# Kernel optimization log

Measured on AMD Instinct MI355X. Metric: run time of the kernel, lower is better.

## Reference

```python
import jax, jax.numpy as jnp
import numpy as np

HIDDEN = 1024


def setup_inputs() -> dict:
    key = jax.random.key(0)
    ks = jax.random.split(key, 8)
    x_in, y_in, out_dim, hidden = 1024, 1024, 1024, HIDDEN
    Nx, Ny = 4096, 4096
    s = lambda d: 1.0 / np.sqrt(d)
    return {
        "x": jax.random.normal(ks[0], (Nx, x_in), jnp.float32),
        "y": jax.random.normal(ks[1], (Ny, y_in), jnp.float32),
        "Wq": jax.random.normal(ks[2], (hidden, x_in), jnp.float32) * s(x_in),
        "bq": jnp.zeros((hidden,), jnp.float32),
        "Wk": jax.random.normal(ks[3], (hidden, y_in), jnp.float32) * s(y_in),
        "bk": jnp.zeros((hidden,), jnp.float32),
        "Wv": jax.random.normal(ks[4], (out_dim, y_in), jnp.float32) * s(y_in),
        "bv": jnp.zeros((out_dim,), jnp.float32),
    }


def reference(x, y, Wq, bq, Wk, bk, Wv, bv):
    # Linear projections (torch Linear: x @ W.T + b)
    q = x @ Wq.T + bq          # [Nx, H]
    k = y @ Wk.T + bk          # [Ny, H]
    v = y @ Wv.T + bv          # [Ny, D_out]
    scores = (q @ k.T) / jnp.sqrt(jnp.asarray(HIDDEN, q.dtype))  # [Nx, Ny]
    attn = jax.nn.softmax(scores, axis=1)
    return attn @ v            # [Nx, D_out]
```

## Files before the change

### kernel.cpp

```cpp
#include <hip/hip_runtime.h>
#include <cstdint>
#include <cstddef>

typedef __attribute__((ext_vector_type(8))) __bf16 bf16x8;
typedef __attribute__((ext_vector_type(4))) float  f32x4;

#define WAITCNT_VM(n) ((n & 0xF) | 0x70 | 0xF00 | (((n) >> 4) << 14))
#define WAITCNT_LGKM0 (0xF | 0x70 | (3 << 14))

__device__ __forceinline__ unsigned short f32_to_bf16(float f) {
    union { float f; unsigned int u; } cv;
    cv.f = f;
    unsigned int u = cv.u;
    return (unsigned short)((u + 0x7fffu + ((u >> 16) & 1u)) >> 16);
}

__device__ __forceinline__ float bf16_to_f32(unsigned short h) {
    union { unsigned int u; float f; } cv;
    cv.u = ((unsigned int)h) << 16;
    return cv.f;
}

__device__ __forceinline__ void async_copy16(const unsigned short* g, unsigned short* lds) {
    __builtin_amdgcn_global_load_lds(
        (const __attribute__((address_space(1))) unsigned int*)g,
        (__attribute__((address_space(3))) unsigned int*)lds,
        16, 0, 0);
}

__global__ __launch_bounds__(256) void cast_all(
    const float* __restrict__ x,  const float* __restrict__ y,
    const float* __restrict__ wq, const float* __restrict__ wk, const float* __restrict__ wv,
    unsigned short* __restrict__ xb,  unsigned short* __restrict__ yb,
    unsigned short* __restrict__ wqb, unsigned short* __restrict__ wkb,
    unsigned short* __restrict__ wvb, float* __restrict__ lsum)
{
    int b = blockIdx.x;
    if (b >= 11264) {
        float4 z = {0.f, 0.f, 0.f, 0.f};
#pragma unroll
        for (int t = 0; t < 4; ++t)
            ((float4*)lsum)[threadIdx.x * 4 + t] = z;
        return;
    }
    const float* s; unsigned short* d; int base;
    if      (b < 4096)  { s = x;  d = xb;  base = b; }
    else if (b < 8192)  { s = y;  d = yb;  base = b - 4096; }
    else if (b < 9216)  { s = wq; d = wqb; base = b - 8192; }
    else if (b < 10240) { s = wk; d = wkb; base = b - 9216; }
    else                { s = wv; d = wvb; base = b - 10240; }
    int i = base * 256 + threadIdx.x;
    float4 v = ((const float4*)s)[i];
    ushort4 o;
    o.x = f32_to_bf16(v.x);
    o.y = f32_to_bf16(v.y);
    o.z = f32_to_bf16(v.z);
    o.w = f32_to_bf16(v.w);
    ((ushort4*)d)[i] = o;
}

__device__ __forceinline__ void gemm_core_pf(
    const unsigned short* __restrict__ A, const unsigned short* __restrict__ B,
    int K, int rowBase, int colBase, int kBeg, int kEnd,
    unsigned short* ldsA, unsigned short* ldsB, f32x4 acc[4][4])
{
    const int tid  = threadIdx.x;
    const int lane = tid & 63;
    const int wave = tid >> 6;
    const int quad = lane >> 4;
    const int r    = lane & 15;
    const int wm   = wave >> 1;
    const int wn   = wave & 1;

    const int c1 = tid + 256;
    const long aOff0 = (long)(rowBase + (tid >> 2)) * K + (tid & 3) * 8;
    const long aOff1 = (long)(rowBase + (c1  >> 2)) * K + (c1  & 3) * 8;
    const long bOff0 = (long)(colBase + (tid >> 2)) * K + (tid & 3) * 8;
    const long bOff1 = (long)(colBase + (c1  >> 2)) * K + (c1  & 3) * 8;
    unsigned short* ldsA0 = ldsA + tid * 8;
    unsigned short* ldsA1 = ldsA + c1 * 8;
    unsigned short* ldsB0 = ldsB + tid * 8;
    unsigned short* ldsB1 = ldsB + c1 * 8;

    const int aReadOff = (wm * 64 + r) * 32 + quad * 8;
    const int bReadOff = (wn * 64 + r) * 32 + quad * 8;

    const int nSteps = (kEnd - kBeg) >> 5;

    async_copy16(A + aOff0 + kBeg, ldsA0);
    async_copy16(A + aOff1 + kBeg, ldsA1);
    async_copy16(B + bOff0 + kBeg, ldsB0);
    async_copy16(B + bOff1 + kBeg, ldsB1);

    for (int s = 0; s < nSteps; ++s) {
        const int cur = (s & 1) << 12;
        const int nxt = cur ^ 4096;
        __builtin_amdgcn_s_waitcnt(0);
        __syncthreads();
        if (s + 1 < nSteps) {
            const int kn = kBeg + ((s + 1) << 5);
            async_copy16(A + aOff0 + kn, ldsA0 + nxt);
            async_copy16(A + aOff1 + kn, ldsA1 + nxt);
            async_copy16(B + bOff0 + kn, ldsB0 + nxt);
            async_copy16(B + bOff1 + kn, ldsB1 + nxt);
        }
        bf16x8 af[4], bfr[4];
#pragma unroll
        for (int i = 0; i < 4; ++i)
            af[i] = *(const bf16x8*)(ldsA + cur + aReadOff + i * 16 * 32);
#pragma unroll
        for (int j = 0; j < 4; ++j)
            bfr[j] = *(const bf16x8*)(ldsB + cur + bReadOff + j * 16 * 32);
#pragma unroll
        for (int i = 0; i < 4; ++i)
#pragma unroll
            for (int j = 0; j < 4; ++j)
                acc[i][j] = __builtin_amdgcn_mfma_f32_16x16x32_bf16(af[i], bfr[j], acc[i][j], 0, 0, 0);
    }
}

__global__ __launch_bounds__(256, 2)
void proj_batched(const unsigned short* __restrict__ xb, const unsigned short* __restrict__ yb,
                  const unsigned short* __restrict__ wqb, const unsigned short* __restrict__ wkb,
                  const unsigned short* __restrict__ wvb,
                  unsigned short* __restrict__ q, unsigned short* __restrict__ k,
                  unsigned short* __restrict__ vt,
                  const float* __restrict__ bq, const float* __restrict__ bk,
                  const float* __restrict__ bv)
{
    __shared__ __align__(16) unsigned short ldsA[2 * 128 * 32];
    __shared__ __align__(16) unsigned short ldsB[2 * 128 * 32];

    const int b = blockIdx.x;
    const int z = b >> 8;
    const int rb = b & 255;

    const unsigned short *A, *B;
    unsigned short* C;
    const float* bias;
    int N, rowBase, colBase;
    bool biasPerRow;
    if (z == 0) {
        A = xb; B = wqb; C = q; bias = bq; N = 1024; biasPerRow = false;
        colBase = (rb >> 5) * 128; rowBase = (rb & 31) * 128;
    } else if (z == 1) {
        A = yb; B = wkb; C = k; bias = bk; N = 1024; biasPerRow = false;
        colBase = (rb >> 5) * 128; rowBase = (rb & 31) * 128;
    } else {
        A = wvb; B = yb; C = vt; bias = bv; N = 4096; biasPerRow = true;
        colBase = (rb >> 3) * 128; rowBase = (rb & 7) * 128;
    }

    f32x4 acc[4][4];
#pragma unroll
    for (int i = 0; i < 4; ++i)
#pragma unroll
        for (int j = 0; j < 4; ++j)
            acc[i][j] = (f32x4){0.f, 0.f, 0.f, 0.f};

    gemm_core_pf(A, B, 1024, rowBase, colBase, 0, 1024, ldsA, ldsB, acc);

    const int lane = threadIdx.x & 63;
    const int wave = threadIdx.x >> 6;
    const int quad = lane >> 4;
    const int r    = lane & 15;
    const int orow0 = rowBase + (wave >> 1) * 64 + quad * 4;
    const int ocol0 = colBase + (wave & 1) * 64 + r;

#pragma unroll
    for (int i = 0; i < 4; ++i)
#pragma unroll
        for (int e = 0; e < 4; ++e) {
            const int row = orow0 + i * 16 + e;
            const float brow = biasPerRow ? bias[row] : 0.f;
#pragma unroll
            for (int j = 0; j < 4; ++j) {
                const int col = ocol0 + j * 16;
                const float bb = biasPerRow ? brow : bias[col];
                C[(long)row * N + col] = f32_to_bf16(acc[i][j][e] + bb);
            }
        }
}

__device__ __forceinline__ void stage_half(const unsigned short* src, long rstep,
                                           unsigned short* ldsLane) {
    async_copy16(src, ldsLane);
    async_copy16(src + rstep, ldsLane + 4096);
}

__device__ __forceinline__ void gemm256_core(
    const unsigned short* __restrict__ A, const unsigned short* __restrict__ B,
    int K, int rowBase, int colBase, int kBeg, int nTiles,
    unsigned short* lds, f32x4 acc[8][4])
{
    const int tid  = threadIdx.x;
    const int lane = tid & 63;
    const int wid  = tid >> 6;
    const int quad = lane >> 4;
    const int r    = lane & 15;
    const int wm   = wid >> 2;
    const int wn   = wid & 3;

    const int row0 = tid >> 3;
    const int chs8 = (((tid & 7) ^ (row0 & 7)) << 3);
    const unsigned short* As = A + (long)(rowBase + row0) * K + chs8 + kBeg;
    const unsigned short* Bs = B + (long)(colBase + row0) * K + chs8 + kBeg;
    const long rstep = (long)K * 64;
    const long hstep = (long)K * 128;
    unsigned short* ldsLane = lds + tid * 8;

    const int aRd = (wm << 13) + (r << 6);
    const int bRd = 16384 + (wn << 12) + (r << 6);
    const int sw0 = ((quad ^ (r & 7)) << 3);
    const int sw1 = (((quad + 4) ^ (r & 7)) << 3);

    stage_half(As,         rstep, ldsLane);
    stage_half(As + hstep, rstep, ldsLane + 8192);
    stage_half(Bs,         rstep, ldsLane + 16384);
    stage_half(Bs + hstep, rstep, ldsLane + 24576);
    if (nTiles > 1) {
        stage_half(As + 64,         rstep, ldsLane + 32768);
        stage_half(As + hstep + 64, rstep, ldsLane + 40960);
    }
    __builtin_amdgcn_s_waitcnt(WAITCNT_VM(4));
    __builtin_amdgcn_s_barrier();
    __builtin_amdgcn_sched_barrier(0);

    for (int T = 0; T < nTiles; ++T) {
        const int cur = (T & 1) << 15;
        const int nxt = cur ^ 32768;

        bf16x8 a0[8], b0[4];
        if (T + 1 < nTiles) stage_half(Bs + (T + 1) * 64, rstep, ldsLane + nxt + 16384);
#pragma unroll
        for (int i = 0; i < 8; ++i)
            a0[i] = *(const bf16x8*)(lds + cur + aRd + i * 1024 + sw0);
#pragma unroll
        for (int j = 0; j < 4; ++j)
            b0[j] = *(const bf16x8*)(lds + cur + bRd + j * 1024 + sw0);
        __builtin_amdgcn_s_barrier();
        __builtin_amdgcn_s_waitcnt(WAITCNT_LGKM0);
        __builtin_amdgcn_sched_barrier(0);
        __builtin_amdgcn_s_setprio(1);
#pragma unroll
        for (int i = 0; i < 4; ++i)
#pragma unroll
            for (int j = 0; j < 4; ++j)
                acc[i][j] = __builtin_amdgcn_mfma_f32_16x16x32_bf16(a0[i], b0[j], acc[i][j], 0, 0, 0);
        __builtin_amdgcn_s_setprio(0);
        __builtin_amdgcn_s_barrier();

        if (T + 1 < nTiles) stage_half(Bs + hstep + (T + 1) * 64, rstep, ldsLane + nxt + 24576);
        __builtin_amdgcn_s_setprio(1);
#pragma unroll
        for (int i = 4; i < 8; ++i)
#pragma unroll
            for (int j = 0; j < 4; ++j)
                acc[i][j] = __builtin_amdgcn_mfma_f32_16x16x32_bf16(a0[i], b0[j], acc[i][j], 0, 0, 0);
        __builtin_amdgcn_s_setprio(0);
        __builtin_amdgcn_s_barrier();

        bf16x8 a1[8], b1[4];
#pragma unroll
        for (int i = 0; i < 8; ++i)
            a1[i] = *(const bf16x8*)(lds + cur + aRd + i * 1024 + sw1);
#pragma unroll
        for (int j = 0; j < 4; ++j)
            b1[j] = *(const bf16x8*)(lds + cur + bRd + j * 1024 + sw1);
        __builtin_amdgcn_s_barrier();
        __builtin_amdgcn_s_waitcnt(WAITCNT_LGKM0);
        __builtin_amdgcn_sched_barrier(0);
        __builtin_amdgcn_s_setprio(1);
#pragma unroll
        for (int i = 0; i < 4; ++i)
#pragma unroll
            for (int j = 0; j < 4; ++j)
                acc[i][j] = __builtin_amdgcn_mfma_f32_16x16x32_bf16(a1[i], b1[j], acc[i][j], 0, 0, 0);
        __builtin_amdgcn_s_setprio(0);
        __builtin_amdgcn_s_barrier();

        if (T + 2 < nTiles) {
            stage_half(As + (T + 2) * 64,         rstep, ldsLane + cur);
            stage_half(As + hstep + (T + 2) * 64, rstep, ldsLane + cur + 8192);
        }
        __builtin_amdgcn_s_setprio(1);
#pragma unroll
        for (int i = 4; i < 8; ++i)
#pragma unroll
            for (int j = 0; j < 4; ++j)
                acc[i][j] = __builtin_amdgcn_mfma_f32_16x16x32_bf16(a1[i], b1[j], acc[i][j], 0, 0, 0);
        __builtin_amdgcn_s_setprio(0);

        if (T + 2 < nTiles) __builtin_amdgcn_s_waitcnt(WAITCNT_VM(4));
        else                __builtin_amdgcn_s_waitcnt(WAITCNT_VM(0));
        __builtin_amdgcn_s_barrier();
        __builtin_amdgcn_sched_barrier(0);
    }
}

__global__ __launch_bounds__(512, 2)
void scores_gemm256(const unsigned short* __restrict__ q, const unsigned short* __restrict__ k,
                    unsigned short* __restrict__ P, float* __restrict__ lsum, float scale2)
{
    __shared__ __align__(16) unsigned short lds[2 * 32768];

    const int bid = blockIdx.x;
    const int swz = (bid & 7) * 32 + (bid >> 3);
    const int mt = swz >> 4, nt = swz & 15;
    const int rowBase = mt * 256;
    const int colBase = nt * 256;

    f32x4 acc[8][4];
#pragma unroll
    for (int i = 0; i < 8; ++i)
#pragma unroll
        for (int j = 0; j < 4; ++j)
            acc[i][j] = (f32x4){0.f, 0.f, 0.f, 0.f};

    gemm256_core(q, k, 1024, rowBase, colBase, 0, 16, lds, acc);

    const int lane = threadIdx.x & 63;
    const int wid  = threadIdx.x >> 6;
    const int quad = lane >> 4;
    const int r    = lane & 15;
    const int orow0 = rowBase + (wid >> 2) * 128 + quad * 4;
    const int ocol0 = colBase + (wid & 3) * 64 + r;

#pragma unroll
    for (int mi = 0; mi < 8; ++mi)
#pragma unroll
        for (int e = 0; e < 4; ++e) {
            const int row = orow0 + mi * 16 + e;
            float rs = 0.f;
#pragma unroll
            for (int nj = 0; nj < 4; ++nj) {
                const float p = exp2f(acc[mi][nj][e] * scale2);
                rs += p;
                P[(long)row * 4096 + ocol0 + nj * 16] = f32_to_bf16(p);
            }
#pragma unroll
            for (int m = 1; m < 16; m <<= 1) rs += __shfl_xor(rs, m, 64);
            if (r == 0) atomicAdd(&lsum[row], rs);
        }
}

template <int ATOMIC>
__global__ __launch_bounds__(512, 2)
void out_gemm256(const unsigned short* __restrict__ P, const unsigned short* __restrict__ vt,
                 void* __restrict__ Out)
{
    __shared__ __align__(16) unsigned short lds[2 * 32768];

    const int bid = blockIdx.x;
    const int swz = (bid & 7) * 32 + (bid >> 3);
    const int z  = swz & 3;
    const int nt = (swz >> 2) & 3;
    const int mt = swz >> 4;
    const int rowBase = mt * 256;
    const int colBase = nt * 256;
    const int kBeg = z * 1024;

    f32x4 acc[8][4];
#pragma unroll
    for (int i = 0; i < 8; ++i)
#pragma unroll
        for (int j = 0; j < 4; ++j)
            acc[i][j] = (f32x4){0.f, 0.f, 0.f, 0.f};

    gemm256_core(P, vt, 4096, rowBase, colBase, kBeg, 16, lds, acc);

    const int lane = threadIdx.x & 63;
    const int wid  = threadIdx.x >> 6;
    const int quad = lane >> 4;
    const int r    = lane & 15;
    const int orow0 = rowBase + (wid >> 2) * 128 + quad * 4;
    const int ocol0 = colBase + (wid & 3) * 64 + r;

#pragma unroll
    for (int mi = 0; mi < 8; ++mi)
#pragma unroll
        for (int e = 0; e < 4; ++e) {
            const int row = orow0 + mi * 16 + e;
#pragma unroll
            for (int nj = 0; nj < 4; ++nj) {
                const int col = ocol0 + nj * 16;
                if (ATOMIC) {
                    atomicAdd(&((float*)Out)[(long)row * 1024 + col], acc[mi][nj][e]);
                } else {
                    unsigned short* parts = (unsigned short*)Out + (size_t)z * (4096 * 1024);
                    parts[(long)row * 1024 + col] = f32_to_bf16(acc[mi][nj][e]);
                }
            }
        }
}

__global__ __launch_bounds__(256) void reduce_norm4(const unsigned short* __restrict__ parts,
                                                    const float* __restrict__ lsum,
                                                    float* __restrict__ O) {
    const int i = blockIdx.x * 256 + threadIdx.x;
    const float inv = 1.0f / lsum[i >> 8];
    const size_t stride = (size_t)(4096 * 1024) / 4;
    ushort4 a = ((const ushort4*)parts)[i];
    ushort4 b = ((const ushort4*)parts)[i + stride];
    ushort4 c = ((const ushort4*)parts)[i + 2 * stride];
    ushort4 d = ((const ushort4*)parts)[i + 3 * stride];
    float4 o;
    o.x = (bf16_to_f32(a.x) + bf16_to_f32(b.x) + bf16_to_f32(c.x) + bf16_to_f32(d.x)) * inv;
    o.y = (bf16_to_f32(a.y) + bf16_to_f32(b.y) + bf16_to_f32(c.y) + bf16_to_f32(d.y)) * inv;
    o.z = (bf16_to_f32(a.z) + bf16_to_f32(b.z) + bf16_to_f32(c.z) + bf16_to_f32(d.z)) * inv;
    o.w = (bf16_to_f32(a.w) + bf16_to_f32(b.w) + bf16_to_f32(c.w) + bf16_to_f32(d.w)) * inv;
    ((float4*)O)[i] = o;
}

__global__ __launch_bounds__(256) void norm_rows(float* __restrict__ O, const float* __restrict__ lsum) {
    int i = blockIdx.x * 256 + threadIdx.x;
    const float inv = 1.0f / lsum[i >> 8];
    float4 v = ((const float4*)O)[i];
    v.x *= inv; v.y *= inv; v.z *= inv; v.w *= inv;
    ((float4*)O)[i] = v;
}

extern "C" void kernel_launch(void* const* d_in, const int* in_sizes, int n_in,
                              void* d_out, int out_size, void* d_ws, size_t ws_size,
                              hipStream_t stream) {
    const float* x  = (const float*)d_in[0];
    const float* y  = (const float*)d_in[1];
    const float* Wq = (const float*)d_in[2];
    const float* bq = (const float*)d_in[3];
    const float* Wk = (const float*)d_in[4];
    const float* bk = (const float*)d_in[5];
    const float* Wv = (const float*)d_in[6];
    const float* bv = (const float*)d_in[7];

    constexpr int Nx = 4096, Ny = 4096, H = 1024, Dv = 1024, Kin = 1024;

    char* ws = (char*)d_ws;
    size_t off = 0;
    auto carve = [&](size_t bytes) {
        char* p = ws + off;
        off += (bytes + 255) & ~(size_t)255;
        return p;
    };

    unsigned short* q_bf  = (unsigned short*)carve((size_t)Nx * H * 2);
    unsigned short* k_bf  = (unsigned short*)carve((size_t)Ny * H * 2);
    unsigned short* vt_bf = (unsigned short*)carve((size_t)Dv * Ny * 2);
    float*          lsum  = (float*)carve((size_t)Nx * sizeof(float));

    char* overlay = ws + off;
    unsigned short* x_bf  = (unsigned short*)overlay;
    unsigned short* y_bf  = x_bf  + (size_t)Nx * Kin;
    unsigned short* Wq_bf = y_bf  + (size_t)Ny * Kin;
    unsigned short* Wk_bf = Wq_bf + (size_t)H  * Kin;
    unsigned short* Wv_bf = Wk_bf + (size_t)H  * Kin;
    unsigned short* P_bf  = (unsigned short*)overlay;

    const size_t overlay_bytes = (size_t)Nx * Ny * 2;
    const size_t partsBytes = (size_t)Nx * Dv * 2;
    unsigned short* parts = (unsigned short*)(overlay + overlay_bytes);
    const size_t need_parts = (size_t)((overlay + overlay_bytes + 4 * partsBytes) - ws);
    const bool useParts = ws_size >= need_parts;

    if (!useParts)
        hipMemsetAsync(d_out, 0, (size_t)Nx * Dv * sizeof(float), stream);

    cast_all<<<11265, 256, 0, stream>>>(x, y, Wq, Wk, Wv, x_bf, y_bf, Wq_bf, Wk_bf, Wv_bf, lsum);

    proj_batched<<<768, 256, 0, stream>>>(x_bf, y_bf, Wq_bf, Wk_bf, Wv_bf,
                                          q_bf, k_bf, vt_bf, bq, bk, bv);

    const float scale2 = 1.4426950408889634f / 32.0f;
    scores_gemm256<<<256, 512, 0, stream>>>(q_bf, k_bf, P_bf, lsum, scale2);

    if (useParts) {
        out_gemm256<0><<<256, 512, 0, stream>>>(P_bf, vt_bf, parts);
        reduce_norm4<<<(Nx * Dv / 4) / 256, 256, 0, stream>>>(parts, lsum, (float*)d_out);
    } else {
        out_gemm256<1><<<256, 512, 0, stream>>>(P_bf, vt_bf, d_out);
        norm_rows<<<Nx * Dv / 4 / 256, 256, 0, stream>>>((float*)d_out, lsum);
    }
}
```

Measured before the change: 223.4 us.

## Restructure GEMM mainloop to overlap LDS fragment reads with MFMA clusters

```diff
diff --git a/kernel.cpp b/kernel.cpp
--- a/kernel.cpp
+++ b/kernel.cpp
@@ -5,8 +5,8 @@
 typedef __attribute__((ext_vector_type(8))) __bf16 bf16x8;
 typedef __attribute__((ext_vector_type(4))) float  f32x4;
 
-#define WAITCNT_VM(n) ((n & 0xF) | 0x70 | 0xF00 | (((n) >> 4) << 14))
-#define WAITCNT_LGKM0 (0xF | 0x70 | (3 << 14))
+#define WAITCNT_VM(n)   ((n & 0xF) | 0x70 | 0xF00 | (((n) >> 4) << 14))
+#define WAITCNT_LGKM(n) (0xF | 0x70 | ((n) << 8) | (3 << 14))
 
 __device__ __forceinline__ unsigned short f32_to_bf16(float f) {
     union { float f; unsigned int u; } cv;
@@ -219,82 +219,101 @@
     stage_half(Bs,         rstep, ldsLane + 16384);
     stage_half(Bs + hstep, rstep, ldsLane + 24576);
     if (nTiles > 1) {
-        stage_half(As + 64,         rstep, ldsLane + 32768);
-        stage_half(As + hstep + 64, rstep, ldsLane + 40960);
+        stage_half(Bs + 64,         rstep, ldsLane + 32768 + 16384);
+        stage_half(Bs + hstep + 64, rstep, ldsLane + 32768 + 24576);
     }
     __builtin_amdgcn_s_waitcnt(WAITCNT_VM(4));
     __builtin_amdgcn_s_barrier();
     __builtin_amdgcn_sched_barrier(0);
 
+    bf16x8 aE[4], aO[4], bX[4], bY[4];
+#pragma unroll
+    for (int i = 0; i < 4; ++i)
+        aE[i] = *(const bf16x8*)(lds + aRd + i * 1024 + sw0);
+#pragma unroll
+    for (int j = 0; j < 4; ++j)
+        bX[j] = *(const bf16x8*)(lds + bRd + j * 1024 + sw0);
+
     for (int T = 0; T < nTiles; ++T) {
         const int cur = (T & 1) << 15;
         const int nxt = cur ^ 32768;
 
-        bf16x8 a0[8], b0[4];
-        if (T + 1 < nTiles) stage_half(Bs + (T + 1) * 64, rstep, ldsLane + nxt + 16384);
-#pragma unroll
-        for (int i = 0; i < 8; ++i)
-            a0[i] = *(const bf16x8*)(lds + cur + aRd + i * 1024 + sw0);
+#pragma unroll
+        for (int i = 0; i < 4; ++i)
+            aO[i] = *(const bf16x8*)(lds + cur + aRd + (4 + i) * 1024 + sw0);
+        __builtin_amdgcn_s_waitcnt(WAITCNT_LGKM(4));
+        __builtin_amdgcn_sched_barrier(0);
+        __builtin_amdgcn_s_setprio(1);
+#pragma unroll
+        for (int i = 0; i < 4; ++i)
+#pragma unroll
+            for (int j = 0; j < 4; ++j)
+                acc[i][j] = __builtin_amdgcn_mfma_f32_16x16x32_bf16(aE[i], bX[j], acc[i][j], 0, 0, 0);
+        __builtin_amdgcn_s_setprio(0);
+        __builtin_amdgcn_sched_barrier(0);
+        __builtin_amdgcn_s_barrier();
+        if (T + 1 < nTiles) stage_half(As + (T + 1) * 64, rstep, ldsLane + nxt);
+
+#pragma unroll
+        for (int i = 0; i < 4; ++i)
+            aE[i] = *(const bf16x8*)(lds + cur + aRd + i * 1024 + sw1);
 #pragma unroll
         for (int j = 0; j < 4; ++j)
-            b0[j] = *(const bf16x8*)(lds + cur + bRd + j * 1024 + sw0);
+            bY[j] = *(const bf16x8*)(lds + cur + bRd + j * 1024 + sw1);
+        __builtin_amdgcn_s_waitcnt(WAITCNT_LGKM(8));
+        __builtin_amdgcn_sched_barrier(0);
+        __builtin_amdgcn_s_setprio(1);
+#pragma unroll
+        for (int i = 0; i < 4; ++i)
+#pragma unroll
+            for (int j = 0; j < 4; ++j)
+                acc[4 + i][j] = __builtin_amdgcn_mfma_f32_16x16x32_bf16(aO[i], bX[j], acc[4 + i][j], 0, 0, 0);
+        __builtin_amdgcn_s_setprio(0);
+        __builtin_amdgcn_sched_barrier(0);
         __builtin_amdgcn_s_barrier();
-        __builtin_amdgcn_s_waitcnt(WAITCNT_LGKM0);
+        if (T + 1 < nTiles) stage_half(As + hstep + (T + 1) * 64, rstep, ldsLane + nxt + 8192);
+
+#pragma unroll
+        for (int i = 0; i < 4; ++i)
+            aO[i] = *(const bf16x8*)(lds + cur + aRd + (4 + i) * 1024 + sw1);
+        __builtin_amdgcn_s_waitcnt(WAITCNT_LGKM(4));
         __builtin_amdgcn_sched_barrier(0);
         __builtin_amdgcn_s_setprio(1);
 #pragma unroll
         for (int i = 0; i < 4; ++i)
 #pragma unroll
             for (int j = 0; j < 4; ++j)
-                acc[i][j] = __builtin_amdgcn_mfma_f32_16x16x32_bf16(a0[i], b0[j], acc[i][j], 0, 0, 0);
+                acc[i][j] = __builtin_amdgcn_mfma_f32_16x16x32_bf16(aE[i], bY[j], acc[i][j], 0, 0, 0);
         __builtin_amdgcn_s_setprio(0);
+        __builtin_amdgcn_sched_barrier(0);
         __builtin_amdgcn_s_barrier();
-
-        if (T + 1 < nTiles) stage_half(Bs + hstep + (T + 1) * 64, rstep, ldsLane + nxt + 24576);
+        if (T + 2 < nTiles) stage_half(Bs + (T + 2) * 64, rstep, ldsLane + cur + 16384);
+
+        if (T + 1 < nTiles) {
+            if (T + 2 < nTiles) __builtin_amdgcn_s_waitcnt(WAITCNT_VM(2));
+            else                __builtin_amdgcn_s_waitcnt(WAITCNT_VM(0));
+            __builtin_amdgcn_s_barrier();
+            __builtin_amdgcn_sched_barrier(0);
+#pragma unroll
+            for (int i = 0; i < 4; ++i)
+                aE[i] = *(const bf16x8*)(lds + nxt + aRd + i * 1024 + sw0);
+#pragma unroll
+            for (int j = 0; j < 4; ++j)
+                bX[j] = *(const bf16x8*)(lds + nxt + bRd + j * 1024 + sw0);
+            __builtin_amdgcn_s_waitcnt(WAITCNT_LGKM(8));
+        } else {
+            __builtin_amdgcn_s_waitcnt(WAITCNT_LGKM(0));
+        }
+        __builtin_amdgcn_sched_barrier(0);
         __builtin_amdgcn_s_setprio(1);
 #pragma unroll
-        for (int i = 4; i < 8; ++i)
+        for (int i = 0; i < 4; ++i)
 #pragma unroll
             for (int j = 0; j < 4; ++j)
-                acc[i][j] = __builtin_amdgcn_mfma_f32_16x16x32_bf16(a0[i], b0[j], acc[i][j], 0, 0, 0);
+                acc[4 + i][j] = __builtin_amdgcn_mfma_f32_16x16x32_bf16(aO[i], bY[j], acc[4 + i][j], 0, 0, 0);
         __builtin_amdgcn_s_setprio(0);
-        __builtin_amdgcn_s_barrier();
-
-        bf16x8 a1[8], b1[4];
-#pragma unroll
-        for (int i = 0; i < 8; ++i)
-            a1[i] = *(const bf16x8*)(lds + cur + aRd + i * 1024 + sw1);
-#pragma unroll
-        for (int j = 0; j < 4; ++j)
-            b1[j] = *(const bf16x8*)(lds + cur + bRd + j * 1024 + sw1);
-        __builtin_amdgcn_s_barrier();
-        __builtin_amdgcn_s_waitcnt(WAITCNT_LGKM0);
-        __builtin_amdgcn_sched_barrier(0);
-        __builtin_amdgcn_s_setprio(1);
-#pragma unroll
-        for (int i = 0; i < 4; ++i)
-#pragma unroll
-            for (int j = 0; j < 4; ++j)
-                acc[i][j] = __builtin_amdgcn_mfma_f32_16x16x32_bf16(a1[i], b1[j], acc[i][j], 0, 0, 0);
-        __builtin_amdgcn_s_setprio(0);
-        __builtin_amdgcn_s_barrier();
-
-        if (T + 2 < nTiles) {
-            stage_half(As + (T + 2) * 64,         rstep, ldsLane + cur);
-            stage_half(As + hstep + (T + 2) * 64, rstep, ldsLane + cur + 8192);
-        }
-        __builtin_amdgcn_s_setprio(1);
-#pragma unroll
-        for (int i = 4; i < 8; ++i)
-#pragma unroll
-            for (int j = 0; j < 4; ++j)
-                acc[i][j] = __builtin_amdgcn_mfma_f32_16x16x32_bf16(a1[i], b1[j], acc[i][j], 0, 0, 0);
-        __builtin_amdgcn_s_setprio(0);
-
-        if (T + 2 < nTiles) __builtin_amdgcn_s_waitcnt(WAITCNT_VM(4));
-        else                __builtin_amdgcn_s_waitcnt(WAITCNT_VM(0));
-        __builtin_amdgcn_s_barrier();
-        __builtin_amdgcn_sched_barrier(0);
+        __builtin_amdgcn_sched_barrier(0);
+        if (T + 2 < nTiles) stage_half(Bs + hstep + (T + 2) * 64, rstep, ldsLane + cur + 24576);
     }
 }
 
```

New measurement: 223.1 us. No clear change (-0.1%).

## Restructure 256-tile GEMM main loop into 8-phase quadrant schedule, 1 block/CU

Applied to the files above, without the earlier changes.

```diff
diff --git a/kernel.cpp b/kernel.cpp
--- a/kernel.cpp
+++ b/kernel.cpp
@@ -5,8 +5,8 @@
 typedef __attribute__((ext_vector_type(8))) __bf16 bf16x8;
 typedef __attribute__((ext_vector_type(4))) float  f32x4;
 
-#define WAITCNT_VM(n) ((n & 0xF) | 0x70 | 0xF00 | (((n) >> 4) << 14))
-#define WAITCNT_LGKM0 (0xF | 0x70 | (3 << 14))
+#define WAITCNT_VM(n)   ((n & 0xF) | 0x70 | 0xF00 | (((n) >> 4) << 14))
+#define WAITCNT_LGKM(n) (0xF | 0x70 | ((n) << 8) | (3 << 14))
 
 __device__ __forceinline__ unsigned short f32_to_bf16(float f) {
     union { float f; unsigned int u; } cv;
@@ -182,12 +182,6 @@
         }
 }
 
-__device__ __forceinline__ void stage_half(const unsigned short* src, long rstep,
-                                           unsigned short* ldsLane) {
-    async_copy16(src, ldsLane);
-    async_copy16(src + rstep, ldsLane + 4096);
-}
-
 __device__ __forceinline__ void gemm256_core(
     const unsigned short* __restrict__ A, const unsigned short* __restrict__ B,
     int K, int rowBase, int colBase, int kBeg, int nTiles,
@@ -209,96 +203,115 @@
     const long hstep = (long)K * 128;
     unsigned short* ldsLane = lds + tid * 8;
 
+    auto STG = [&](const unsigned short* src, int ldsOff) {
+        async_copy16(src,         ldsLane + ldsOff);
+        async_copy16(src + rstep, ldsLane + ldsOff + 4096);
+    };
+
     const int aRd = (wm << 13) + (r << 6);
     const int bRd = 16384 + (wn << 12) + (r << 6);
     const int sw0 = ((quad ^ (r & 7)) << 3);
     const int sw1 = (((quad + 4) ^ (r & 7)) << 3);
 
-    stage_half(As,         rstep, ldsLane);
-    stage_half(As + hstep, rstep, ldsLane + 8192);
-    stage_half(Bs,         rstep, ldsLane + 16384);
-    stage_half(Bs + hstep, rstep, ldsLane + 24576);
-    if (nTiles > 1) {
-        stage_half(As + 64,         rstep, ldsLane + 32768);
-        stage_half(As + hstep + 64, rstep, ldsLane + 40960);
+#define G256_RD_A(arr, bufOff, mo) \
+    { _Pragma("unroll") for (int m = 0; m < 4; ++m) { \
+        arr[m]     = *(const bf16x8*)(lds + (bufOff) + aRd + ((mo) + m) * 1024 + sw0); \
+        arr[4 + m] = *(const bf16x8*)(lds + (bufOff) + aRd + ((mo) + m) * 1024 + sw1); } }
+#define G256_RD_B(arr, bufOff, no) \
+    { _Pragma("unroll") for (int n = 0; n < 2; ++n) { \
+        arr[n]     = *(const bf16x8*)(lds + (bufOff) + bRd + ((no) + n) * 1024 + sw0); \
+        arr[2 + n] = *(const bf16x8*)(lds + (bufOff) + bRd + ((no) + n) * 1024 + sw1); } }
+#define G256_MFMA(mb, nb, Af, Bf) \
+    { _Pragma("unroll") for (int kq = 0; kq < 2; ++kq) \
+      _Pragma("unroll") for (int m = 0; m < 4; ++m) \
+      _Pragma("unroll") for (int n = 0; n < 2; ++n) \
+        acc[(mb) + m][(nb) + n] = __builtin_amdgcn_mfma_f32_16x16x32_bf16( \
+            Af[kq * 4 + m], Bf[kq * 2 + n], acc[(mb) + m][(nb) + n], 0, 0, 0); }
+#define G256_BAR  __builtin_amdgcn_s_barrier()
+#define G256_LG0  __builtin_amdgcn_s_waitcnt(WAITCNT_LGKM(0))
+#define G256_SB   __builtin_amdgcn_sched_barrier(0)
+#define G256_PR1  __builtin_amdgcn_s_setprio(1)
+#define G256_PR0  __builtin_amdgcn_s_setprio(0)
+#define G256_VM_TAIL(cond) \
+    { if (cond) __builtin_amdgcn_s_waitcnt(WAITCNT_VM(4)); \
+      else      __builtin_amdgcn_s_waitcnt(WAITCNT_VM(0)); }
+
+    STG(As,         0);
+    STG(As + hstep, 8192);
+    STG(Bs,         16384);
+    STG(Bs + hstep, 24576);
+    STG(As + 64,         32768);
+    STG(As + 64 + hstep, 40960);
+    __builtin_amdgcn_s_waitcnt(WAITCNT_VM(4));
+    G256_BAR;
+    G256_SB;
+
+    bf16x8 aLo[8], aHi[8], bLo[4], bHi[4];
+    const int nIt = nTiles >> 1;
+    for (int i = 0; i < nIt; ++i) {
+        const int t1 = 2 * i + 1, t2 = 2 * i + 2, t3 = 2 * i + 3;
+        const bool s2 = t2 < nTiles, s3 = t3 < nTiles;
+
+        G256_RD_A(aLo, 0, 0); G256_RD_B(bLo, 0, 0);
+        STG(Bs + t1 * 64, 32768 + 16384);
+        G256_BAR; G256_LG0; G256_SB;
+        G256_PR1; G256_MFMA(0, 0, aLo, bLo); G256_PR0;
+        G256_BAR;
+
+        G256_RD_A(aHi, 0, 4);
+        STG(Bs + t1 * 64 + hstep, 32768 + 24576);
+        G256_BAR; G256_LG0; G256_SB;
+        G256_PR1; G256_MFMA(4, 0, aHi, bLo); G256_PR0;
+        G256_BAR;
+
+        G256_RD_B(bHi, 0, 2);
+        if (s2) STG(As + t2 * 64, 0);
+        G256_BAR; G256_LG0; G256_SB;
+        G256_PR1; G256_MFMA(4, 2, aHi, bHi); G256_PR0;
+        G256_BAR;
+
+        if (s2) STG(As + t2 * 64 + hstep, 8192);
+        G256_VM_TAIL(s2);
+        G256_BAR; G256_SB;
+        G256_PR1; G256_MFMA(0, 2, aLo, bHi); G256_PR0;
+        G256_BAR;
+
+        G256_RD_A(aLo, 32768, 0); G256_RD_B(bLo, 32768, 0);
+        if (s2) STG(Bs + t2 * 64, 16384);
+        G256_BAR; G256_LG0; G256_SB;
+        G256_PR1; G256_MFMA(0, 0, aLo, bLo); G256_PR0;
+        G256_BAR;
+
+        G256_RD_A(aHi, 32768, 4);
+        if (s2) STG(Bs + t2 * 64 + hstep, 24576);
+        G256_BAR; G256_LG0; G256_SB;
+        G256_PR1; G256_MFMA(4, 0, aHi, bLo); G256_PR0;
+        G256_BAR;
+
+        G256_RD_B(bHi, 32768, 2);
+        if (s3) STG(As + t3 * 64, 32768);
+        G256_BAR; G256_LG0; G256_SB;
+        G256_PR1; G256_MFMA(4, 2, aHi, bHi); G256_PR0;
+        G256_BAR;
+
+        if (s3) STG(As + t3 * 64 + hstep, 32768 + 8192);
+        G256_VM_TAIL(s3);
+        G256_BAR; G256_SB;
+        G256_PR1; G256_MFMA(0, 2, aLo, bHi); G256_PR0;
+        G256_BAR;
     }
-    __builtin_amdgcn_s_waitcnt(WAITCNT_VM(4));
-    __builtin_amdgcn_s_barrier();
-    __builtin_amdgcn_sched_barrier(0);
-
-    for (int T = 0; T < nTiles; ++T) {
-        const int cur = (T & 1) << 15;
-        const int nxt = cur ^ 32768;
-
-        bf16x8 a0[8], b0[4];
-        if (T + 1 < nTiles) stage_half(Bs + (T + 1) * 64, rstep, ldsLane + nxt + 16384);
-#pragma unroll
-        for (int i = 0; i < 8; ++i)
-            a0[i] = *(const bf16x8*)(lds + cur + aRd + i * 1024 + sw0);
-#pragma unroll
-        for (int j = 0; j < 4; ++j)
-            b0[j] = *(const bf16x8*)(lds + cur + bRd + j * 1024 + sw0);
-        __builtin_amdgcn_s_barrier();
-        __builtin_amdgcn_s_waitcnt(WAITCNT_LGKM0);
-        __builtin_amdgcn_sched_barrier(0);
-        __builtin_amdgcn_s_setprio(1);
-#pragma unroll
-        for (int i = 0; i < 4; ++i)
-#pragma unroll
-            for (int j = 0; j < 4; ++j)
-                acc[i][j] = __builtin_amdgcn_mfma_f32_16x16x32_bf16(a0[i], b0[j], acc[i][j], 0, 0, 0);
-        __builtin_amdgcn_s_setprio(0);
-        __builtin_amdgcn_s_barrier();
-
-        if (T + 1 < nTiles) stage_half(Bs + hstep + (T + 1) * 64, rstep, ldsLane + nxt + 24576);
-        __builtin_amdgcn_s_setprio(1);
-#pragma unroll
-        for (int i = 4; i < 8; ++i)
-#pragma unroll
-            for (int j = 0; j < 4; ++j)
-                acc[i][j] = __builtin_amdgcn_mfma_f32_16x16x32_bf16(a0[i], b0[j], acc[i][j], 0, 0, 0);
-        __builtin_amdgcn_s_setprio(0);
-        __builtin_amdgcn_s_barrier();
-
-        bf16x8 a1[8], b1[4];
-#pragma unroll
-        for (int i = 0; i < 8; ++i)
-            a1[i] = *(const bf16x8*)(lds + cur + aRd + i * 1024 + sw1);
-#pragma unroll
-        for (int j = 0; j < 4; ++j)
-            b1[j] = *(const bf16x8*)(lds + cur + bRd + j * 1024 + sw1);
-        __builtin_amdgcn_s_barrier();
-        __builtin_amdgcn_s_waitcnt(WAITCNT_LGKM0);
-        __builtin_amdgcn_sched_barrier(0);
-        __builtin_amdgcn_s_setprio(1);
-#pragma unroll
-        for (int i = 0; i < 4; ++i)
-#pragma unroll
-            for (int j = 0; j < 4; ++j)
-                acc[i][j] = __builtin_amdgcn_mfma_f32_16x16x32_bf16(a1[i], b1[j], acc[i][j], 0, 0, 0);
-        __builtin_amdgcn_s_setprio(0);
-        __builtin_amdgcn_s_barrier();
-
-        if (T + 2 < nTiles) {
-            stage_half(As + (T + 2) * 64,         rstep, ldsLane + cur);
-            stage_half(As + hstep + (T + 2) * 64, rstep, ldsLane + cur + 8192);
-        }
-        __builtin_amdgcn_s_setprio(1);
-#pragma unroll
-        for (int i = 4; i < 8; ++i)
-#pragma unroll
-            for (int j = 0; j < 4; ++j)
-                acc[i][j] = __builtin_amdgcn_mfma_f32_16x16x32_bf16(a1[i], b1[j], acc[i][j], 0, 0, 0);
-        __builtin_amdgcn_s_setprio(0);
-
-        if (T + 2 < nTiles) __builtin_amdgcn_s_waitcnt(WAITCNT_VM(4));
-        else                __builtin_amdgcn_s_waitcnt(WAITCNT_VM(0));
-        __builtin_amdgcn_s_barrier();
-        __builtin_amdgcn_sched_barrier(0);
-    }
-}
-
-__global__ __launch_bounds__(512, 2)
+#undef G256_RD_A
+#undef G256_RD_B
+#undef G256_MFMA
+#undef G256_BAR
+#undef G256_LG0
+#undef G256_SB
+#undef G256_PR1
+#undef G256_PR0
+#undef G256_VM_TAIL
+}
+
+__global__ __launch_bounds__(512, 1)
 void scores_gemm256(const unsigned short* __restrict__ q, const unsigned short* __restrict__ k,
                     unsigned short* __restrict__ P, float* __restrict__ lsum, float scale2)
 {
@@ -345,7 +358,7 @@
 }
 
 template <int ATOMIC>
-__global__ __launch_bounds__(512, 2)
+__global__ __launch_bounds__(512, 1)
 void out_gemm256(const unsigned short* __restrict__ P, const unsigned short* __restrict__ vt,
                  void* __restrict__ Out)
 {
```

Measured after the change: 223.3 us. No clear change (-0.0%).
